# Kernel optimization log

Hardware: AMD Instinct MI355X
Metric: run time of the kernel (lower is better)

Reference implementation:

```python
import jax, jax.numpy as jnp
import numpy as np

D_MODEL = 1024
N_HEADS = 16
D_HEAD = D_MODEL // N_HEADS
D_FF = 4096
BATCH = 2
SEQ = 2048
EPS = 1e-5


def setup_inputs() -> dict:
    key = jax.random.key(0)
    ks = jax.random.split(key, 8)
    s = 0.02
    x = jax.random.normal(ks[0], (BATCH, SEQ, D_MODEL), dtype=jnp.float32)
    # Per-head projection weights, stacked: [H, d_head, d_model] (torch Linear stores (out,in))
    wq = jax.random.normal(ks[1], (N_HEADS, D_HEAD, D_MODEL), dtype=jnp.float32) * s
    wk = jax.random.normal(ks[2], (N_HEADS, D_HEAD, D_MODEL), dtype=jnp.float32) * s
    wv = jax.random.normal(ks[3], (N_HEADS, D_HEAD, D_MODEL), dtype=jnp.float32) * s
    wo = jax.random.normal(ks[4], (D_MODEL, D_MODEL), dtype=jnp.float32) * s
    w1 = jax.random.normal(ks[5], (D_FF, D_MODEL), dtype=jnp.float32) * s
    w2 = jax.random.normal(ks[6], (D_MODEL, D_FF), dtype=jnp.float32) * s
    ln1_g = jnp.ones((D_MODEL,), jnp.float32)
    ln1_b = jnp.zeros((D_MODEL,), jnp.float32)
    ln2_g = jnp.ones((D_MODEL,), jnp.float32)
    ln2_b = jnp.zeros((D_MODEL,), jnp.float32)
    return {"x": x, "wq": wq, "wk": wk, "wv": wv, "wo": wo,
            "w1": w1, "w2": w2, "ln1_g": ln1_g, "ln1_b": ln1_b,
            "ln2_g": ln2_g, "ln2_b": ln2_b}


def _layer_norm(x, g, b):
    mu = jnp.mean(x, axis=-1, keepdims=True)
    var = jnp.mean(jnp.square(x - mu), axis=-1, keepdims=True)
    return (x - mu) * jax.lax.rsqrt(var + EPS) * g + b


def _mha(h, wq, wk, wv, wo):
    # h: [b,s,d]; wq/wk/wv: [H,dh,d] -> q/k/v: [b,H,s,dh]
    q = jnp.einsum('bsd,hed->bhse', h, wq)
    k = jnp.einsum('bsd,hed->bhse', h, wk)
    v = jnp.einsum('bsd,hed->bhse', h, wv)
    scores = jnp.einsum('bhqe,bhke->bhqk', q, k) / jnp.sqrt(jnp.float32(D_HEAD))
    weights = jax.nn.softmax(scores, axis=-1)
    ctx = jnp.einsum('bhqk,bhke->bhqe', weights, v)  # [b,H,s,dh]
    # concat heads in order (head 0 first) -> [b,s,H*dh]
    concat = jnp.transpose(ctx, (0, 2, 1, 3)).reshape(h.shape[0], h.shape[1], D_MODEL)
    return concat @ wo.T


def reference(x, wq, wk, wv, wo, w1, w2, ln1_g, ln1_b, ln2_g, ln2_b):
    h = _layer_norm(x, ln1_g, ln1_b)
    attn_out = _mha(h, wq, wk, wv, wo)
    h2 = _layer_norm(x + attn_out, ln2_g, ln2_b)
    ff = jax.nn.gelu(h2 @ w1.T, approximate=False) @ w2.T
    return x + ff
```

## Files before the change

kernel.cpp:

```cpp
#include <hip/hip_runtime.h>
#include <hip/hip_bf16.h>
#include <math.h>

typedef __bf16 bf16_t;
typedef __bf16 bf16x8 __attribute__((ext_vector_type(8)));
typedef __bf16 bf16x4 __attribute__((ext_vector_type(4)));
typedef float f32x4 __attribute__((ext_vector_type(4)));
typedef unsigned int u32;
typedef u32 u32x2 __attribute__((ext_vector_type(2)));

#define DM 1024
#define SEQL 2048
#define NTOK 4096
#define QKVN 3072

__device__ __forceinline__ void gload_lds16(const bf16_t* g, bf16_t* l){
  __builtin_amdgcn_global_load_lds((const __attribute__((address_space(1))) void*)g,
                                   (__attribute__((address_space(3))) void*)l, 16, 0, 0);
}
__device__ __forceinline__ u32 ldsoff(const void* p){
  return (u32)(size_t)(__attribute__((address_space(3))) const void*)p;
}
__device__ __forceinline__ u32x2 tr64(u32 byte_off){
  u32x2 d;
  asm volatile("ds_read_b64_tr_b16 %0, %1" : "=v"(d) : "v"(byte_off));
  return d;
}
__device__ __forceinline__ u32 pack2(float a, float b){
  union{ __bf16 h[2]; u32 w; } z;
  z.h[0]=(__bf16)a; z.h[1]=(__bf16)b; return z.w;
}

__global__ __launch_bounds__(256) void cvt_kernel(const float* __restrict__ src,
    bf16_t* __restrict__ dst, int n)
{
  const int i = (blockIdx.x*256 + threadIdx.x)*4;
  if (i < n){
    const float4 v = *(const float4*)(src + i);
    bf16x4 o; o[0]=(__bf16)v.x; o[1]=(__bf16)v.y; o[2]=(__bf16)v.z; o[3]=(__bf16)v.w;
    *(bf16x4*)(dst + i) = o;
  }
}

__global__ __launch_bounds__(256) void ln_kernel(const float* __restrict__ in,
    const float* __restrict__ g, const float* __restrict__ bta,
    bf16_t* __restrict__ outp)
{
  const int row = blockIdx.x;
  const int t = threadIdx.x;
  const float4 v = *(const float4*)(in + (size_t)row*DM + t*4);
  float s  = v.x+v.y+v.z+v.w;
  float sq = v.x*v.x+v.y*v.y+v.z*v.z+v.w*v.w;
  #pragma unroll
  for (int m=1;m<64;m<<=1){ s += __shfl_xor(s,m); sq += __shfl_xor(sq,m); }
  __shared__ float red[8];
  const int w = t>>6;
  if ((t&63)==0){ red[w]=s; red[4+w]=sq; }
  __syncthreads();
  s  = red[0]+red[1]+red[2]+red[3];
  sq = red[4]+red[5]+red[6]+red[7];
  const float mean = s*(1.f/DM);
  const float var  = sq*(1.f/DM) - mean*mean;
  const float rstd = rsqrtf(var + 1e-5f);
  const float4 gg = *(const float4*)(g + t*4);
  const float4 bb = *(const float4*)(bta + t*4);
  bf16x4 o;
  o[0]=(__bf16)((v.x-mean)*rstd*gg.x+bb.x);
  o[1]=(__bf16)((v.y-mean)*rstd*gg.y+bb.y);
  o[2]=(__bf16)((v.z-mean)*rstd*gg.z+bb.z);
  o[3]=(__bf16)((v.w-mean)*rstd*gg.w+bb.w);
  *(bf16x4*)(outp + (size_t)row*DM + t*4) = o;
}

template<int EPI>
__global__ __launch_bounds__(512, 2) void gemm256(
    const bf16_t* __restrict__ A, const bf16_t* __restrict__ Bw,
    void* __restrict__ Cout, int N, int K)
{
  constexpr int BK = 32;
  __shared__ __align__(16) char ldsb[3*32768];
  const int tid = threadIdx.x, lane = tid&63, wid = tid>>6;
  const int q16 = lane&15, g = lane>>4;
  const int wm = wid>>2, wn = wid&3;

  const int flat = blockIdx.y*gridDim.x + blockIdx.x;
  const int xcd = flat&7, j = flat>>3;
  const int NY = gridDim.y;
  const int jdiv = j/NY, jmod = j - jdiv*NY;
  const int bm = (xcd*2 + jdiv)*256, bn = jmod*256;

  int mloc, kloc;
  {
    const u32 L = tid*16;
    const u32 logical = L ^ (((L>>9)&1)<<5);
    mloc = (int)((logical>>10)*16 + ((logical&1023)>>6));
    kloc = (int)((logical&63)>>1);
  }
  const bf16_t* asrc[2]; const bf16_t* bsrc[2];
  #pragma unroll
  for (int ht=0; ht<2; ht++){
    asrc[ht] = A  + (size_t)(bm + ht*128 + mloc)*K + kloc;
    bsrc[ht] = Bw + (size_t)(bn + ht*128 + mloc)*K + kloc;
  }
  const u32 laneOff = ((u32)(q16*64 + g*16)) ^ ((u32)(q16&8)<<2);

  f32x4 acc[8][4] = {};

  auto stageA = [&](int buf, int ht, int k0){
    gload_lds16(asrc[ht] + k0, (bf16_t*)(ldsb + buf*32768 + ht*8192 + tid*16));
  };
  auto stageB = [&](int buf, int ht, int k0){
    gload_lds16(bsrc[ht] + k0, (bf16_t*)(ldsb + buf*32768 + 16384 + ht*8192 + tid*16));
  };

  stageA(0,0,0); stageA(0,1,0); stageB(0,0,0); stageB(0,1,0);
  stageA(1,0,BK); stageA(1,1,BK); stageB(1,0,BK); stageB(1,1,BK);
  asm volatile("s_waitcnt vmcnt(4)" ::: "memory");
  __builtin_amdgcn_s_barrier();

  const int NT = K/BK;
  int bcur = 0;
  for (int kt=0; kt<NT; kt++){
    const int bstg = (bcur >= 1) ? bcur-1 : bcur+2;
    const char* Ab = ldsb + bcur*32768 + wm*8192;
    const char* Bb = ldsb + bcur*32768 + 16384 + (wn>>1)*8192;
    const bool sOK = (kt+2 < NT);
    const int k0s = (kt+2)*BK;
    bf16x8 bv[4];
    #pragma unroll
    for (int p=0; p<2; p++){
      bf16x8 av[4];
      #pragma unroll
      for (int jx=0;jx<4;jx++)
        av[jx] = *(const bf16x8*)(Ab + ((p*4+jx)<<10) + laneOff);
      if (p==0){
        #pragma unroll
        for (int jx=0;jx<4;jx++)
          bv[jx] = *(const bf16x8*)(Bb + ((((wn&1)*4)+jx)<<10) + laneOff);
      }
      if (sOK){
        if (p==0){ stageA(bstg,0,k0s); stageA(bstg,1,k0s); }
        else     { stageB(bstg,0,k0s); stageB(bstg,1,k0s); }
      }
      asm volatile("s_barrier" ::: "memory");
      __builtin_amdgcn_s_setprio(1);
      #pragma unroll
      for (int jx=0;jx<4;jx++)
        #pragma unroll
        for (int j2=0;j2<4;j2++)
          acc[p*4+jx][j2] = __builtin_amdgcn_mfma_f32_16x16x32_bf16(av[jx], bv[j2], acc[p*4+jx][j2], 0,0,0);
      __builtin_amdgcn_s_setprio(0);
      if (p==1){
        if (sOK) asm volatile("s_waitcnt vmcnt(4)" ::: "memory");
        else     asm volatile("s_waitcnt vmcnt(0)" ::: "memory");
      }
      asm volatile("s_barrier" ::: "memory");
    }
    bcur = (bcur==2)?0:bcur+1;
  }

  #pragma unroll
  for (int fm=0; fm<8; fm++)
    #pragma unroll
    for (int fn=0; fn<4; fn++)
      #pragma unroll
      for (int i=0; i<4; i++){
        const int r = bm + wm*128 + fm*16 + g*4 + i;
        const int c = bn + wn*64 + fn*16 + q16;
        const size_t idx = (size_t)r*N + c;
        const float vv = acc[fm][fn][i];
        if constexpr (EPI==0){
          ((bf16_t*)Cout)[idx] = (__bf16)vv;
        } else {
          const float ge = 0.5f*vv*(1.0f + erff(vv*0.70710678118654752f));
          ((bf16_t*)Cout)[idx] = (__bf16)ge;
        }
      }
}

__global__ __launch_bounds__(512, 2) void gemm128(
    const bf16_t* __restrict__ A, const bf16_t* __restrict__ Bw,
    float* __restrict__ Cout, const float* __restrict__ X,
    int N, int K)
{
  constexpr int BK = 32;
  __shared__ __align__(16) char ldsb[3*16384];
  const int tid = threadIdx.x, lane = tid&63, wid = tid>>6;
  const int q16 = lane&15, g = lane>>4;
  const int wm = wid>>2, wn = wid&3;

  const int flat = blockIdx.y*gridDim.x + blockIdx.x;
  const int xcd = flat&7, j = flat>>3;
  const int bm = ((xcd<<2) + (j>>3))*128, bn = (j&7)*128;

  int mloc, kloc;
  {
    const u32 L = tid*16;
    const u32 logical = L ^ (((L>>9)&1)<<5);
    mloc = (int)((logical>>10)*16 + ((logical&1023)>>6));
    kloc = (int)((logical&63)>>1);
  }
  const bf16_t* asrc = A  + (size_t)(bm + mloc)*K + kloc;
  const bf16_t* bsrc = Bw + (size_t)(bn + mloc)*K + kloc;
  const u32 laneOff = ((u32)(q16*64 + g*16)) ^ ((u32)(q16&8)<<2);

  f32x4 acc[4][2] = {};

  auto stageA = [&](int buf, int k0){
    gload_lds16(asrc + k0, (bf16_t*)(ldsb + buf*16384 + tid*16));
  };
  auto stageB = [&](int buf, int k0){
    gload_lds16(bsrc + k0, (bf16_t*)(ldsb + buf*16384 + 8192 + tid*16));
  };

  stageA(0,0); stageB(0,0);
  stageA(1,BK); stageB(1,BK);
  asm volatile("s_waitcnt vmcnt(2)" ::: "memory");
  __builtin_amdgcn_s_barrier();

  const int NT = K/BK;
  int bcur = 0;
  for (int kt=0; kt<NT; kt++){
    const int bstg = (bcur >= 1) ? bcur-1 : bcur+2;
    const char* Ab = ldsb + bcur*16384 + wm*4096;
    const char* Bb = ldsb + bcur*16384 + 8192 + wn*2048;
    const bool sOK = (kt+2 < NT);
    const int k0s = (kt+2)*BK;
    bf16x8 bv[2];
    #pragma unroll
    for (int p=0; p<2; p++){
      bf16x8 av[2];
      #pragma unroll
      for (int jx=0;jx<2;jx++)
        av[jx] = *(const bf16x8*)(Ab + ((p*2+jx)<<10) + laneOff);
      if (p==0){
        #pragma unroll
        for (int jx=0;jx<2;jx++)
          bv[jx] = *(const bf16x8*)(Bb + (jx<<10) + laneOff);
      }
      if (sOK){
        if (p==0) stageA(bstg,k0s);
        else      stageB(bstg,k0s);
      }
      asm volatile("s_barrier" ::: "memory");
      __builtin_amdgcn_s_setprio(1);
      #pragma unroll
      for (int jx=0;jx<2;jx++)
        #pragma unroll
        for (int j2=0;j2<2;j2++)
          acc[p*2+jx][j2] = __builtin_amdgcn_mfma_f32_16x16x32_bf16(av[jx], bv[j2], acc[p*2+jx][j2], 0,0,0);
      __builtin_amdgcn_s_setprio(0);
      if (p==1){
        if (sOK) asm volatile("s_waitcnt vmcnt(2)" ::: "memory");
        else     asm volatile("s_waitcnt vmcnt(0)" ::: "memory");
      }
      asm volatile("s_barrier" ::: "memory");
    }
    bcur = (bcur==2)?0:bcur+1;
  }

  #pragma unroll
  for (int fm=0; fm<4; fm++)
    #pragma unroll
    for (int fn=0; fn<2; fn++)
      #pragma unroll
      for (int i=0; i<4; i++){
        const int r = bm + wm*64 + fm*16 + g*4 + i;
        const int c = bn + wn*32 + fn*16 + q16;
        const size_t idx = (size_t)r*N + c;
        Cout[idx] = X[idx] + acc[fm][fn][i];
      }
}

__global__ __launch_bounds__(512, 4) void attn_kernel(
    const bf16_t* __restrict__ QKV, bf16_t* __restrict__ Ctx)
{
  __shared__ __align__(16) bf16_t Ks[2][64*64];
  __shared__ __align__(16) bf16_t Vs[2][16*4*72];
  const int tid = threadIdx.x, lane = tid&63, w = tid>>6;
  const int g = lane>>4, q16 = lane&15;
  const int bh = blockIdx.y, b = bh>>4, h = bh&15;
  const int qr0 = blockIdx.x*128 + w*16;
  const size_t tok0 = (size_t)b*SEQL;
  const int ch0 = h*64;

  bf16x8 aq[2];
  #pragma unroll
  for (int ks=0; ks<2; ks++){
    bf16x8 t = *(const bf16x8*)(QKV + (tok0+qr0+q16)*QKVN + ch0 + ks*32 + g*8);
    #pragma unroll
    for (int jx=0;jx<8;jx++) t[jx] = (__bf16)((float)t[jx]*0.125f);
    aq[ks] = t;
  }

  const int srow = tid>>3, sc8 = (tid&7)*8;
  const bf16_t* kptr = QKV + (tok0+srow)*QKVN + 1024 + ch0 + sc8;
  const bf16_t* vptr = kptr + 1024;
  const int kwoff = srow*64 + (sc8 ^ ((srow&7)<<3));
  const int vwoff = ((srow>>2)*4 + (sc8>>4))*72 + (srow&3)*16 + (sc8&15);

  float mrun = -1e30f, lrun = 0.f;
  f32x4 o[4] = {};

  bf16x8 kreg = *(const bf16x8*)kptr;
  bf16x8 vreg = *(const bf16x8*)vptr;
  *(bf16x8*)&Ks[0][kwoff] = kreg;
  *(bf16x8*)&Vs[0][vwoff] = vreg;
  kreg = *(const bf16x8*)(kptr + (size_t)64*QKVN);
  vreg = *(const bf16x8*)(vptr + (size_t)64*QKVN);

  const int NT = SEQL/64;
  for (int t=0; t<NT; t++){
    __syncthreads();
    if (t+1 < NT){
      *(bf16x8*)&Ks[(t+1)&1][kwoff] = kreg;
      *(bf16x8*)&Vs[(t+1)&1][vwoff] = vreg;
      if (t+2 < NT){
        kreg = *(const bf16x8*)(kptr + (size_t)(t+2)*64*QKVN);
        vreg = *(const bf16x8*)(vptr + (size_t)(t+2)*64*QKVN);
      }
    }
    const bf16_t* ksb = Ks[t&1];
    const u32 vs0 = ldsoff(&Vs[t&1][0]);

    f32x4 s[4] = {};
    #pragma unroll
    for (int ks=0; ks<2; ks++){
      #pragma unroll
      for (int fn=0; fn<4; fn++){
        const int r = fn*16 + q16;
        const int ce = ks*32 + g*8;
        bf16x8 bk = *(const bf16x8*)&ksb[r*64 + (ce ^ ((r&7)<<3))];
        s[fn] = __builtin_amdgcn_mfma_f32_16x16x32_bf16(bk, aq[ks], s[fn], 0, 0, 0);
      }
    }

    float m0 = fmaxf(fmaxf(s[0][0],s[0][1]), fmaxf(s[0][2],s[0][3]));
    float m1 = fmaxf(fmaxf(s[1][0],s[1][1]), fmaxf(s[1][2],s[1][3]));
    float m2 = fmaxf(fmaxf(s[2][0],s[2][1]), fmaxf(s[2][2],s[2][3]));
    float m3 = fmaxf(fmaxf(s[3][0],s[3][1]), fmaxf(s[3][2],s[3][3]));
    float mx = fmaxf(fmaxf(m0,m1), fmaxf(m2,m3));
    mx = fmaxf(mx, __shfl_xor(mx,16));
    mx = fmaxf(mx, __shfl_xor(mx,32));

    if (!__all(mx <= mrun + 8.0f)){
      const float mnew = fmaxf(mrun, mx);
      const float alpha = __expf(mrun - mnew);
      #pragma unroll
      for (int i=0;i<4;i++){
        const float ai = __shfl(alpha, g*4+i);
        o[0][i]*=ai; o[1][i]*=ai; o[2][i]*=ai; o[3][i]*=ai;
      }
      lrun *= alpha;
      mrun = mnew;
    }

    float rs = 0.f;
    u32 u[4][2];
    #pragma unroll
    for (int fn=0; fn<4; fn++){
      const float e0=__expf(s[fn][0]-mrun), e1=__expf(s[fn][1]-mrun);
      const float e2=__expf(s[fn][2]-mrun), e3=__expf(s[fn][3]-mrun);
      rs += (e0+e1)+(e2+e3);
      u[fn][0] = pack2(e0,e1);
      u[fn][1] = pack2(e2,e3);
    }
    rs += __shfl_xor(rs,16);
    rs += __shfl_xor(rs,32);
    lrun += rs;

    #pragma unroll
    for (int ks=0; ks<2; ks++){
      u32x2 vlo[4], vhi[4];
      #pragma unroll
      for (int ne=0; ne<4; ne++){
        const u32 vb = vs0 + (u32)((((ks*8 + 2*g)*4 + ne)*72 + q16)*2);
        vlo[ne] = tr64(vb);
        vhi[ne] = tr64(vb + 576);
      }
      union { u32 wd[4]; bf16x8 v; } pa;
      #pragma unroll
      for (int jj=0; jj<4; jj++){
        const int src = q16 + ((((g&1)<<1) + (jj>>1))<<4);
        const u32 a0 = (u32)__shfl((int)u[2*ks  ][jj&1], src);
        const u32 a1 = (u32)__shfl((int)u[2*ks+1][jj&1], src);
        pa.wd[jj] = (g&2) ? a1 : a0;
      }
      asm volatile("s_waitcnt lgkmcnt(0)" ::: "memory");
      __builtin_amdgcn_sched_barrier(0);
      union { u32x2 u2[2]; bf16x8 v; } cc;
      #pragma unroll
      for (int ne=0; ne<4; ne++){
        cc.u2[0]=vlo[ne]; cc.u2[1]=vhi[ne];
        o[ne] = __builtin_amdgcn_mfma_f32_16x16x32_bf16(pa.v, cc.v, o[ne], 0, 0, 0);
      }
    }
  }

  const float rl = 1.0f/lrun;
  #pragma unroll
  for (int i=0; i<4; i++){
    const float ri = __shfl(rl, g*4+i);
    #pragma unroll
    for (int ne=0; ne<4; ne++){
      const int r = qr0 + g*4 + i;
      Ctx[(tok0+r)*DM + ch0 + ne*16 + q16] = (__bf16)(o[ne][i]*ri);
    }
  }
}

extern "C" void kernel_launch(void* const* d_in, const int* in_sizes, int n_in,
                              void* d_out, int out_size, void* d_ws, size_t ws_size,
                              hipStream_t stream)
{
  (void)in_sizes; (void)n_in; (void)out_size; (void)ws_size;
  const float* x  = (const float*)d_in[0];
  const float* wq = (const float*)d_in[1];
  const float* wk = (const float*)d_in[2];
  const float* wv = (const float*)d_in[3];
  const float* wo = (const float*)d_in[4];
  const float* w1 = (const float*)d_in[5];
  const float* w2 = (const float*)d_in[6];
  const float* g1 = (const float*)d_in[7];
  const float* b1 = (const float*)d_in[8];
  const float* g2 = (const float*)d_in[9];
  const float* b2 = (const float*)d_in[10];
  float* out = (float*)d_out;
  char* ws = (char*)d_ws;
  const size_t MB = 1024ull*1024ull;

  bf16_t* wqkv_b = (bf16_t*)(ws);
  bf16_t* wo_b   = (bf16_t*)(ws + 6*MB);
  bf16_t* w1_b   = (bf16_t*)(ws + 8*MB);
  bf16_t* w2_b   = (bf16_t*)(ws + 16*MB);
  bf16_t* h1     = (bf16_t*)(ws + 24*MB);
  bf16_t* qkv    = (bf16_t*)(ws + 32*MB);
  bf16_t* ctx    = (bf16_t*)(ws + 56*MB);
  float*  res2   = (float*)(ws + 64*MB);
  bf16_t* h2     = h1;
  bf16_t* ffm    = (bf16_t*)(ws + 32*MB);

  cvt_kernel<<<1024, 256, 0, stream>>>(wq, wqkv_b,             1024*1024);
  cvt_kernel<<<1024, 256, 0, stream>>>(wk, wqkv_b + 1024*1024, 1024*1024);
  cvt_kernel<<<1024, 256, 0, stream>>>(wv, wqkv_b + 2048*1024, 1024*1024);
  cvt_kernel<<<1024, 256, 0, stream>>>(wo, wo_b, 1024*1024);
  cvt_kernel<<<4096, 256, 0, stream>>>(w1, w1_b, 4096*1024);
  cvt_kernel<<<4096, 256, 0, stream>>>(w2, w2_b, 4096*1024);

  ln_kernel<<<NTOK, 256, 0, stream>>>(x, g1, b1, h1);
  gemm256<0><<<dim3(16, 12), 512, 0, stream>>>(h1, wqkv_b, (void*)qkv, QKVN, 1024);
  attn_kernel<<<dim3(16, 32), 512, 0, stream>>>(qkv, ctx);
  gemm128<<<dim3(32, 8), 512, 0, stream>>>(ctx, wo_b, res2, x, 1024, 1024);
  ln_kernel<<<NTOK, 256, 0, stream>>>(res2, g2, b2, h2);
  gemm256<2><<<dim3(16, 16), 512, 0, stream>>>(h2, w1_b, (void*)ffm, 4096, 1024);
  gemm128<<<dim3(32, 8), 512, 0, stream>>>(ffm, w2_b, out, x, 1024, 4096);
}
```

Before: 261.0 us.

## Fuse weight conversion and first layernorm; widen attention KV tiles to 128 with exp2

Merges the six weight-conversion launches and the first layernorm into a single prep kernel, so launch overhead and tail gaps between small kernels go away. The attention kernel now processes 128 keys per iteration instead of 64, doubling the LDS buffers and halving the loop trip count and barriers. It also folds log2(e) into the Q scale so exp2f replaces __expf. Larger tiles raise register and LDS pressure, which may lower occupancy under the 512x4 launch bound.

```diff
diff --git a/kernel.cpp b/kernel.cpp
--- a/kernel.cpp
+++ b/kernel.cpp
@@ -31,14 +31,60 @@
   z.h[0]=(__bf16)a; z.h[1]=(__bf16)b; return z.w;
 }
 
-__global__ __launch_bounds__(256) void cvt_kernel(const float* __restrict__ src,
-    bf16_t* __restrict__ dst, int n)
+__global__ __launch_bounds__(256) void prep_kernel(
+    const float* __restrict__ wq, const float* __restrict__ wk,
+    const float* __restrict__ wv, const float* __restrict__ wo,
+    const float* __restrict__ w1, const float* __restrict__ w2,
+    const float* __restrict__ x,  const float* __restrict__ g1,
+    const float* __restrict__ b1,
+    bf16_t* __restrict__ wqkv_b, bf16_t* __restrict__ wo_b,
+    bf16_t* __restrict__ w1_b,   bf16_t* __restrict__ w2_b,
+    bf16_t* __restrict__ h1)
 {
-  const int i = (blockIdx.x*256 + threadIdx.x)*4;
-  if (i < n){
-    const float4 v = *(const float4*)(src + i);
+  __shared__ float red[8];
+  const int bid = blockIdx.x;
+  const int t = threadIdx.x;
+  if (bid < 12288){
+    const int flat = (bid*256 + t)*4;
+    const int seg = flat >> 20;
+    const int off1m = flat & 1048575;
+    const float* src; bf16_t* dst;
+    if (seg < 3){
+      src = (seg==0 ? wq : (seg==1 ? wk : wv)) + off1m;
+      dst = wqkv_b + flat;
+    } else if (seg == 3){
+      src = wo + off1m;  dst = wo_b + off1m;
+    } else if (seg < 8){
+      src = w1 + (flat - 4*1048576);  dst = w1_b + (flat - 4*1048576);
+    } else {
+      src = w2 + (flat - 8*1048576);  dst = w2_b + (flat - 8*1048576);
+    }
+    const float4 v = *(const float4*)src;
     bf16x4 o; o[0]=(__bf16)v.x; o[1]=(__bf16)v.y; o[2]=(__bf16)v.z; o[3]=(__bf16)v.w;
-    *(bf16x4*)(dst + i) = o;
+    *(bf16x4*)dst = o;
+  } else {
+    const int row = bid - 12288;
+    const float4 v = *(const float4*)(x + (size_t)row*DM + t*4);
+    float s  = v.x+v.y+v.z+v.w;
+    float sq = v.x*v.x+v.y*v.y+v.z*v.z+v.w*v.w;
+    #pragma unroll
+    for (int m=1;m<64;m<<=1){ s += __shfl_xor(s,m); sq += __shfl_xor(sq,m); }
+    const int w = t>>6;
+    if ((t&63)==0){ red[w]=s; red[4+w]=sq; }
+    __syncthreads();
+    s  = red[0]+red[1]+red[2]+red[3];
+    sq = red[4]+red[5]+red[6]+red[7];
+    const float mean = s*(1.f/DM);
+    const float var  = sq*(1.f/DM) - mean*mean;
+    const float rstd = rsqrtf(var + 1e-5f);
+    const float4 gg = *(const float4*)(g1 + t*4);
+    const float4 bb = *(const float4*)(b1 + t*4);
+    bf16x4 o;
+    o[0]=(__bf16)((v.x-mean)*rstd*gg.x+bb.x);
+    o[1]=(__bf16)((v.y-mean)*rstd*gg.y+bb.y);
+    o[2]=(__bf16)((v.z-mean)*rstd*gg.z+bb.z);
+    o[3]=(__bf16)((v.w-mean)*rstd*gg.w+bb.w);
+    *(bf16x4*)(h1 + (size_t)row*DM + t*4) = o;
   }
 }
 
@@ -275,8 +321,8 @@
 __global__ __launch_bounds__(512, 4) void attn_kernel(
     const bf16_t* __restrict__ QKV, bf16_t* __restrict__ Ctx)
 {
-  __shared__ __align__(16) bf16_t Ks[2][64*64];
-  __shared__ __align__(16) bf16_t Vs[2][16*4*72];
+  __shared__ __align__(16) bf16_t Ks[2][128*64];
+  __shared__ __align__(16) bf16_t Vs[2][32*4*72];
   const int tid = threadIdx.x, lane = tid&63, w = tid>>6;
   const int g = lane>>4, q16 = lane&15;
   const int bh = blockIdx.y, b = bh>>4, h = bh&15;
@@ -289,7 +335,7 @@
   for (int ks=0; ks<2; ks++){
     bf16x8 t = *(const bf16x8*)(QKV + (tok0+qr0+q16)*QKVN + ch0 + ks*32 + g*8);
     #pragma unroll
-    for (int jx=0;jx<8;jx++) t[jx] = (__bf16)((float)t[jx]*0.125f);
+    for (int jx=0;jx<8;jx++) t[jx] = (__bf16)((float)t[jx]*0.18033688f);
     aq[ks] = t;
   }
 
@@ -302,32 +348,48 @@
   float mrun = -1e30f, lrun = 0.f;
   f32x4 o[4] = {};
 
-  bf16x8 kreg = *(const bf16x8*)kptr;
-  bf16x8 vreg = *(const bf16x8*)vptr;
-  *(bf16x8*)&Ks[0][kwoff] = kreg;
-  *(bf16x8*)&Vs[0][vwoff] = vreg;
-  kreg = *(const bf16x8*)(kptr + (size_t)64*QKVN);
-  vreg = *(const bf16x8*)(vptr + (size_t)64*QKVN);
-
-  const int NT = SEQL/64;
+  bf16x8 kreg[2], vreg[2];
+  #pragma unroll
+  for (int it=0; it<2; it++){
+    kreg[it] = *(const bf16x8*)(kptr + (size_t)it*64*QKVN);
+    vreg[it] = *(const bf16x8*)(vptr + (size_t)it*64*QKVN);
+  }
+  #pragma unroll
+  for (int it=0; it<2; it++){
+    *(bf16x8*)&Ks[0][kwoff + it*4096] = kreg[it];
+    *(bf16x8*)&Vs[0][vwoff + it*4608] = vreg[it];
+  }
+  #pragma unroll
+  for (int it=0; it<2; it++){
+    kreg[it] = *(const bf16x8*)(kptr + (size_t)(128 + it*64)*QKVN);
+    vreg[it] = *(const bf16x8*)(vptr + (size_t)(128 + it*64)*QKVN);
+  }
+
+  const int NT = SEQL/128;
   for (int t=0; t<NT; t++){
     __syncthreads();
     if (t+1 < NT){
-      *(bf16x8*)&Ks[(t+1)&1][kwoff] = kreg;
-      *(bf16x8*)&Vs[(t+1)&1][vwoff] = vreg;
+      #pragma unroll
+      for (int it=0; it<2; it++){
+        *(bf16x8*)&Ks[(t+1)&1][kwoff + it*4096] = kreg[it];
+        *(bf16x8*)&Vs[(t+1)&1][vwoff + it*4608] = vreg[it];
+      }
       if (t+2 < NT){
-        kreg = *(const bf16x8*)(kptr + (size_t)(t+2)*64*QKVN);
-        vreg = *(const bf16x8*)(vptr + (size_t)(t+2)*64*QKVN);
+        #pragma unroll
+        for (int it=0; it<2; it++){
+          kreg[it] = *(const bf16x8*)(kptr + (size_t)((t+2)*128 + it*64)*QKVN);
+          vreg[it] = *(const bf16x8*)(vptr + (size_t)((t+2)*128 + it*64)*QKVN);
+        }
       }
     }
     const bf16_t* ksb = Ks[t&1];
     const u32 vs0 = ldsoff(&Vs[t&1][0]);
 
-    f32x4 s[4] = {};
+    f32x4 s[8] = {};
     #pragma unroll
     for (int ks=0; ks<2; ks++){
       #pragma unroll
-      for (int fn=0; fn<4; fn++){
+      for (int fn=0; fn<8; fn++){
         const int r = fn*16 + q16;
         const int ce = ks*32 + g*8;
         bf16x8 bk = *(const bf16x8*)&ksb[r*64 + (ce ^ ((r&7)<<3))];
@@ -335,17 +397,16 @@
       }
     }
 
-    float m0 = fmaxf(fmaxf(s[0][0],s[0][1]), fmaxf(s[0][2],s[0][3]));
-    float m1 = fmaxf(fmaxf(s[1][0],s[1][1]), fmaxf(s[1][2],s[1][3]));
-    float m2 = fmaxf(fmaxf(s[2][0],s[2][1]), fmaxf(s[2][2],s[2][3]));
-    float m3 = fmaxf(fmaxf(s[3][0],s[3][1]), fmaxf(s[3][2],s[3][3]));
-    float mx = fmaxf(fmaxf(m0,m1), fmaxf(m2,m3));
+    float mx = -1e30f;
+    #pragma unroll
+    for (int fn=0; fn<8; fn++)
+      mx = fmaxf(mx, fmaxf(fmaxf(s[fn][0],s[fn][1]), fmaxf(s[fn][2],s[fn][3])));
     mx = fmaxf(mx, __shfl_xor(mx,16));
     mx = fmaxf(mx, __shfl_xor(mx,32));
 
-    if (!__all(mx <= mrun + 8.0f)){
+    if (!__all(mx <= mrun + 11.54f)){
       const float mnew = fmaxf(mrun, mx);
-      const float alpha = __expf(mrun - mnew);
+      const float alpha = exp2f(mrun - mnew);
       #pragma unroll
       for (int i=0;i<4;i++){
         const float ai = __shfl(alpha, g*4+i);
@@ -356,11 +417,11 @@
     }
 
     float rs = 0.f;
-    u32 u[4][2];
-    #pragma unroll
-    for (int fn=0; fn<4; fn++){
-      const float e0=__expf(s[fn][0]-mrun), e1=__expf(s[fn][1]-mrun);
-      const float e2=__expf(s[fn][2]-mrun), e3=__expf(s[fn][3]-mrun);
+    u32 u[8][2];
+    #pragma unroll
+    for (int fn=0; fn<8; fn++){
+      const float e0=exp2f(s[fn][0]-mrun), e1=exp2f(s[fn][1]-mrun);
+      const float e2=exp2f(s[fn][2]-mrun), e3=exp2f(s[fn][3]-mrun);
       rs += (e0+e1)+(e2+e3);
       u[fn][0] = pack2(e0,e1);
       u[fn][1] = pack2(e2,e3);
@@ -370,7 +431,7 @@
     lrun += rs;
 
     #pragma unroll
-    for (int ks=0; ks<2; ks++){
+    for (int ks=0; ks<4; ks++){
       u32x2 vlo[4], vhi[4];
       #pragma unroll
       for (int ne=0; ne<4; ne++){
@@ -440,14 +501,8 @@
   bf16_t* h2     = h1;
   bf16_t* ffm    = (bf16_t*)(ws + 32*MB);
 
-  cvt_kernel<<<1024, 256, 0, stream>>>(wq, wqkv_b,             1024*1024);
-  cvt_kernel<<<1024, 256, 0, stream>>>(wk, wqkv_b + 1024*1024, 1024*1024);
-  cvt_kernel<<<1024, 256, 0, stream>>>(wv, wqkv_b + 2048*1024, 1024*1024);
-  cvt_kernel<<<1024, 256, 0, stream>>>(wo, wo_b, 1024*1024);
-  cvt_kernel<<<4096, 256, 0, stream>>>(w1, w1_b, 4096*1024);
-  cvt_kernel<<<4096, 256, 0, stream>>>(w2, w2_b, 4096*1024);
-
-  ln_kernel<<<NTOK, 256, 0, stream>>>(x, g1, b1, h1);
+  prep_kernel<<<16384, 256, 0, stream>>>(wq, wk, wv, wo, w1, w2, x, g1, b1,
+                                         wqkv_b, wo_b, w1_b, w2_b, h1);
   gemm256<0><<<dim3(16, 12), 512, 0, stream>>>(h1, wqkv_b, (void*)qkv, QKVN, 1024);
   attn_kernel<<<dim3(16, 32), 512, 0, stream>>>(qkv, ctx);
   gemm128<<<dim3(32, 8), 512, 0, stream>>>(ctx, wo_b, res2, x, 1024, 1024);
```

New measurement: 257.3 us. About the same (-1.4%).

## Merge weight conversion and first LayerNorm into one kernel; restructure 256 GEMM pipeline

Applied to the files above, without the earlier changes.

Six weight-conversion launches and the first LayerNorm are folded into one prep kernel, dispatched by block index, which removes launch gaps. The 256x256 GEMM is rebuilt as an 8-phase schedule over two 64-deep K buffers (128KB LDS) with a simpler row mapping, staging half-tiles across phases to overlap loads with MFMA. The row-mapping change is also applied to gemm128. The larger LDS footprint may limit occupancy, and the hand-written vmcnt/barrier schedule is fragile.

```diff
diff --git a/kernel.cpp b/kernel.cpp
--- a/kernel.cpp
+++ b/kernel.cpp
@@ -31,14 +31,60 @@
   z.h[0]=(__bf16)a; z.h[1]=(__bf16)b; return z.w;
 }
 
-__global__ __launch_bounds__(256) void cvt_kernel(const float* __restrict__ src,
-    bf16_t* __restrict__ dst, int n)
-{
-  const int i = (blockIdx.x*256 + threadIdx.x)*4;
-  if (i < n){
-    const float4 v = *(const float4*)(src + i);
+__global__ __launch_bounds__(256) void prep_kernel(
+    const float* __restrict__ wq, const float* __restrict__ wk,
+    const float* __restrict__ wv, const float* __restrict__ wo,
+    const float* __restrict__ w1, const float* __restrict__ w2,
+    const float* __restrict__ x,  const float* __restrict__ g1,
+    const float* __restrict__ b1,
+    bf16_t* __restrict__ wqkv_b, bf16_t* __restrict__ wo_b,
+    bf16_t* __restrict__ w1_b,   bf16_t* __restrict__ w2_b,
+    bf16_t* __restrict__ h1)
+{
+  __shared__ float red[8];
+  const int bid = blockIdx.x;
+  const int t = threadIdx.x;
+  if (bid < 12288){
+    const int flat = (bid*256 + t)*4;
+    const int seg = flat >> 20;
+    const int off1m = flat & 1048575;
+    const float* src; bf16_t* dst;
+    if (seg < 3){
+      src = (seg==0 ? wq : (seg==1 ? wk : wv)) + off1m;
+      dst = wqkv_b + flat;
+    } else if (seg == 3){
+      src = wo + off1m;  dst = wo_b + off1m;
+    } else if (seg < 8){
+      src = w1 + (flat - 4*1048576);  dst = w1_b + (flat - 4*1048576);
+    } else {
+      src = w2 + (flat - 8*1048576);  dst = w2_b + (flat - 8*1048576);
+    }
+    const float4 v = *(const float4*)src;
     bf16x4 o; o[0]=(__bf16)v.x; o[1]=(__bf16)v.y; o[2]=(__bf16)v.z; o[3]=(__bf16)v.w;
-    *(bf16x4*)(dst + i) = o;
+    *(bf16x4*)dst = o;
+  } else {
+    const int row = bid - 12288;
+    const float4 v = *(const float4*)(x + (size_t)row*DM + t*4);
+    float s  = v.x+v.y+v.z+v.w;
+    float sq = v.x*v.x+v.y*v.y+v.z*v.z+v.w*v.w;
+    #pragma unroll
+    for (int m=1;m<64;m<<=1){ s += __shfl_xor(s,m); sq += __shfl_xor(sq,m); }
+    const int w = t>>6;
+    if ((t&63)==0){ red[w]=s; red[4+w]=sq; }
+    __syncthreads();
+    s  = red[0]+red[1]+red[2]+red[3];
+    sq = red[4]+red[5]+red[6]+red[7];
+    const float mean = s*(1.f/DM);
+    const float var  = sq*(1.f/DM) - mean*mean;
+    const float rstd = rsqrtf(var + 1e-5f);
+    const float4 gg = *(const float4*)(g1 + t*4);
+    const float4 bb = *(const float4*)(b1 + t*4);
+    bf16x4 o;
+    o[0]=(__bf16)((v.x-mean)*rstd*gg.x+bb.x);
+    o[1]=(__bf16)((v.y-mean)*rstd*gg.y+bb.y);
+    o[2]=(__bf16)((v.z-mean)*rstd*gg.z+bb.z);
+    o[3]=(__bf16)((v.w-mean)*rstd*gg.w+bb.w);
+    *(bf16x4*)(h1 + (size_t)row*DM + t*4) = o;
   }
 }
 
@@ -73,91 +119,86 @@
 }
 
 template<int EPI>
-__global__ __launch_bounds__(512, 2) void gemm256(
+__global__ __launch_bounds__(512, 2) void gemm8ph(
     const bf16_t* __restrict__ A, const bf16_t* __restrict__ Bw,
     void* __restrict__ Cout, int N, int K)
 {
-  constexpr int BK = 32;
-  __shared__ __align__(16) char ldsb[3*32768];
+  __shared__ __align__(16) char ldsb[131072];
   const int tid = threadIdx.x, lane = tid&63, wid = tid>>6;
   const int q16 = lane&15, g = lane>>4;
   const int wm = wid>>2, wn = wid&3;
 
   const int flat = blockIdx.y*gridDim.x + blockIdx.x;
-  const int xcd = flat&7, j = flat>>3;
+  const int xcd = flat&7, jj = flat>>3;
   const int NY = gridDim.y;
-  const int jdiv = j/NY, jmod = j - jdiv*NY;
+  const int jdiv = jj/NY, jmod = jj - jdiv*NY;
   const int bm = (xcd*2 + jdiv)*256, bn = jmod*256;
 
   int mloc, kloc;
   {
     const u32 L = tid*16;
     const u32 logical = L ^ (((L>>9)&1)<<5);
-    mloc = (int)((logical>>10)*16 + ((logical&1023)>>6));
+    mloc = (int)(logical>>6);
     kloc = (int)((logical&63)>>1);
   }
-  const bf16_t* asrc[2]; const bf16_t* bsrc[2];
-  #pragma unroll
-  for (int ht=0; ht<2; ht++){
-    asrc[ht] = A  + (size_t)(bm + ht*128 + mloc)*K + kloc;
-    bsrc[ht] = Bw + (size_t)(bn + ht*128 + mloc)*K + kloc;
-  }
+  const bf16_t* asrc = A  + (size_t)(bm + mloc)*K + kloc;
+  const bf16_t* bsrc = Bw + (size_t)(bn + mloc)*K + kloc;
   const u32 laneOff = ((u32)(q16*64 + g*16)) ^ ((u32)(q16&8)<<2);
 
   f32x4 acc[8][4] = {};
-
-  auto stageA = [&](int buf, int ht, int k0){
-    gload_lds16(asrc[ht] + k0, (bf16_t*)(ldsb + buf*32768 + ht*8192 + tid*16));
+  bf16x8 bv[4];
+
+  auto stage = [&](int buf, int kh, int isB, int s){
+    const bf16_t* src = isB ? bsrc : asrc;
+    #pragma unroll
+    for (int h2=0; h2<2; h2++)
+      gload_lds16(src + (size_t)(h2*128)*K + s*64 + kh*32,
+                  (bf16_t*)(ldsb + buf*65536 + isB*32768 + kh*16384 + h2*8192 + tid*16));
   };
-  auto stageB = [&](int buf, int ht, int k0){
-    gload_lds16(bsrc[ht] + k0, (bf16_t*)(ldsb + buf*32768 + 16384 + ht*8192 + tid*16));
-  };
-
-  stageA(0,0,0); stageA(0,1,0); stageB(0,0,0); stageB(0,1,0);
-  stageA(1,0,BK); stageA(1,1,BK); stageB(1,0,BK); stageB(1,1,BK);
+
+  stage(0,0,0,0); stage(0,0,1,0); stage(0,1,0,0); stage(0,1,1,0);
+  stage(1,0,0,1); stage(1,0,1,1);
   asm volatile("s_waitcnt vmcnt(4)" ::: "memory");
   __builtin_amdgcn_s_barrier();
 
-  const int NT = K/BK;
-  int bcur = 0;
-  for (int kt=0; kt<NT; kt++){
-    const int bstg = (bcur >= 1) ? bcur-1 : bcur+2;
-    const char* Ab = ldsb + bcur*32768 + wm*8192;
-    const char* Bb = ldsb + bcur*32768 + 16384 + (wn>>1)*8192;
-    const bool sOK = (kt+2 < NT);
-    const int k0s = (kt+2)*BK;
-    bf16x8 bv[4];
-    #pragma unroll
-    for (int p=0; p<2; p++){
-      bf16x8 av[4];
-      #pragma unroll
-      for (int jx=0;jx<4;jx++)
-        av[jx] = *(const bf16x8*)(Ab + ((p*4+jx)<<10) + laneOff);
-      if (p==0){
-        #pragma unroll
-        for (int jx=0;jx<4;jx++)
-          bv[jx] = *(const bf16x8*)(Bb + ((((wn&1)*4)+jx)<<10) + laneOff);
-      }
-      if (sOK){
-        if (p==0){ stageA(bstg,0,k0s); stageA(bstg,1,k0s); }
-        else     { stageB(bstg,0,k0s); stageB(bstg,1,k0s); }
-      }
-      asm volatile("s_barrier" ::: "memory");
-      __builtin_amdgcn_s_setprio(1);
-      #pragma unroll
-      for (int jx=0;jx<4;jx++)
-        #pragma unroll
-        for (int j2=0;j2<4;j2++)
-          acc[p*4+jx][j2] = __builtin_amdgcn_mfma_f32_16x16x32_bf16(av[jx], bv[j2], acc[p*4+jx][j2], 0,0,0);
-      __builtin_amdgcn_s_setprio(0);
-      if (p==1){
-        if (sOK) asm volatile("s_waitcnt vmcnt(4)" ::: "memory");
-        else     asm volatile("s_waitcnt vmcnt(0)" ::: "memory");
-      }
-      asm volatile("s_barrier" ::: "memory");
-    }
-    bcur = (bcur==2)?0:bcur+1;
-  }
+  const int NSTEP = K>>6;
+  const int NIT = NSTEP>>1;
+
+#define PHASE(BUF,KH,MH,DOST,SBUF,SKH,SISB,SSTEP,CK) { \
+    bf16x8 av[4]; \
+    const char* Ab_ = ldsb + (BUF)*65536 + (KH)*16384 + wm*8192; \
+    _Pragma("unroll") for (int jx=0;jx<4;jx++) \
+      av[jx] = *(const bf16x8*)(Ab_ + (((MH)*4+jx)<<10) + laneOff); \
+    if ((MH)==0){ \
+      const char* Bb_ = ldsb + (BUF)*65536 + 32768 + (KH)*16384 + (wn>>1)*8192; \
+      _Pragma("unroll") for (int jx=0;jx<4;jx++) \
+        bv[jx] = *(const bf16x8*)(Bb_ + ((((wn&1)*4)+jx)<<10) + laneOff); \
+    } \
+    if (DOST) stage(SBUF,SKH,SISB,SSTEP); \
+    asm volatile("s_barrier" ::: "memory"); \
+    asm volatile("s_waitcnt lgkmcnt(0)" ::: "memory"); \
+    __builtin_amdgcn_s_setprio(1); \
+    _Pragma("unroll") for (int jx=0;jx<4;jx++) \
+      _Pragma("unroll") for (int j2=0;j2<4;j2++) \
+        acc[(MH)*4+jx][j2] = __builtin_amdgcn_mfma_f32_16x16x32_bf16(av[jx], bv[j2], acc[(MH)*4+jx][j2],0,0,0); \
+    __builtin_amdgcn_s_setprio(0); \
+    if (CK){ if (nl) { asm volatile("s_waitcnt vmcnt(4)" ::: "memory"); } \
+             else    { asm volatile("s_waitcnt vmcnt(0)" ::: "memory"); } } \
+    asm volatile("s_barrier" ::: "memory"); }
+
+  for (int it=0; it<NIT; it++){
+    const int s0 = 2*it, s1 = s0+1;
+    const bool nl = (it+1 < NIT);
+    PHASE(0,0,0, 1,  1,1,0, s1,   0)
+    PHASE(0,0,1, 1,  1,1,1, s1,   0)
+    PHASE(0,1,0, nl, 0,0,0, s0+2, 0)
+    PHASE(0,1,1, nl, 0,0,1, s0+2, 1)
+    PHASE(1,0,0, nl, 0,1,0, s0+2, 0)
+    PHASE(1,0,1, nl, 0,1,1, s0+2, 0)
+    PHASE(1,1,0, nl, 1,0,0, s1+2, 0)
+    PHASE(1,1,1, nl, 1,0,1, s1+2, 1)
+  }
+#undef PHASE
 
   #pragma unroll
   for (int fm=0; fm<8; fm++)
@@ -197,7 +238,7 @@
   {
     const u32 L = tid*16;
     const u32 logical = L ^ (((L>>9)&1)<<5);
-    mloc = (int)((logical>>10)*16 + ((logical&1023)>>6));
+    mloc = (int)(logical>>6);
     kloc = (int)((logical&63)>>1);
   }
   const bf16_t* asrc = A  + (size_t)(bm + mloc)*K + kloc;
@@ -440,18 +481,12 @@
   bf16_t* h2     = h1;
   bf16_t* ffm    = (bf16_t*)(ws + 32*MB);
 
-  cvt_kernel<<<1024, 256, 0, stream>>>(wq, wqkv_b,             1024*1024);
-  cvt_kernel<<<1024, 256, 0, stream>>>(wk, wqkv_b + 1024*1024, 1024*1024);
-  cvt_kernel<<<1024, 256, 0, stream>>>(wv, wqkv_b + 2048*1024, 1024*1024);
-  cvt_kernel<<<1024, 256, 0, stream>>>(wo, wo_b, 1024*1024);
-  cvt_kernel<<<4096, 256, 0, stream>>>(w1, w1_b, 4096*1024);
-  cvt_kernel<<<4096, 256, 0, stream>>>(w2, w2_b, 4096*1024);
-
-  ln_kernel<<<NTOK, 256, 0, stream>>>(x, g1, b1, h1);
-  gemm256<0><<<dim3(16, 12), 512, 0, stream>>>(h1, wqkv_b, (void*)qkv, QKVN, 1024);
+  prep_kernel<<<16384, 256, 0, stream>>>(wq, wk, wv, wo, w1, w2, x, g1, b1,
+                                         wqkv_b, wo_b, w1_b, w2_b, h1);
+  gemm8ph<0><<<dim3(16, 12), 512, 0, stream>>>(h1, wqkv_b, (void*)qkv, QKVN, 1024);
   attn_kernel<<<dim3(16, 32), 512, 0, stream>>>(qkv, ctx);
   gemm128<<<dim3(32, 8), 512, 0, stream>>>(ctx, wo_b, res2, x, 1024, 1024);
   ln_kernel<<<NTOK, 256, 0, stream>>>(res2, g2, b2, h2);
-  gemm256<2><<<dim3(16, 16), 512, 0, stream>>>(h2, w1_b, (void*)ffm, 4096, 1024);
+  gemm8ph<2><<<dim3(16, 16), 512, 0, stream>>>(h2, w1_b, (void*)ffm, 4096, 1024);
   gemm128<<<dim3(32, 8), 512, 0, stream>>>(ffm, w2_b, out, x, 1024, 4096);
 }
```

Result: faster. 247.2 us (-5.3%).
